# Optimization experiments

Hardware: AMD Instinct MI355X
Metric: run time of the kernel (lower is better)

The kernel has to match this reference:

```python
import jax, jax.numpy as jnp
import numpy as np

B, T, D, H = 4, 2048, 1024, 64

def setup_inputs() -> dict:
    key = jax.random.key(0)
    kx, kq, kk, kv = jax.random.split(key, 4)
    s = 1.0 / np.sqrt(D)
    return {
        "x": jax.random.normal(kx, (B, T, D), dtype=jnp.float32),
        "Wq": jax.random.normal(kq, (D, H), dtype=jnp.float32) * s,
        "Wk": jax.random.normal(kk, (D, H), dtype=jnp.float32) * s,
        "Wv": jax.random.normal(kv, (D, H), dtype=jnp.float32) * s,
    }

def reference(x, Wq, Wk, Wv):
    # q,k,v: [B,T,H]
    q = jnp.einsum('btd,dh->bth', x, Wq)
    k = jnp.einsum('btd,dh->bth', x, Wk)
    v = jnp.einsum('btd,dh->bth', x, Wv)
    scale = jnp.asarray(H, x.dtype) ** -0.5
    wei = jnp.einsum('bqh,bkh->bqk', q, k) * scale  # [B,T,T]
    Tlen = x.shape[1]
    causal = jnp.tril(jnp.ones((Tlen, Tlen), dtype=bool))
    wei = jnp.where(causal, wei, -jnp.inf)
    attn = jax.nn.softmax(wei, axis=-1)
    return jnp.einsum('bqk,bkh->bqh', attn, v)
```

## Files before the change

kernel.cpp:

```cpp
#include <hip/hip_runtime.h>
#include <hip/hip_bf16.h>
#include <math.h>

#define Bb   4
#define Tlen 2048
#define Dd   1024
#define Hh   64
#define NROWS 8192
#define NQ   32
#define NC   4

typedef short bf16x8 __attribute__((ext_vector_type(8)));
typedef float f32x4  __attribute__((ext_vector_type(4)));

__device__ __forceinline__ unsigned short f2b(float f) {
    unsigned u = __float_as_uint(f);
    unsigned r = u + 0x7FFFu + ((u >> 16) & 1u);
    return (unsigned short)(r >> 16);
}
__device__ __forceinline__ unsigned pk2(float a, float b) {
    __hip_bfloat162 h = __float22bfloat162_rn(make_float2(a, b));
    return *reinterpret_cast<unsigned*>(&h);
}

__global__ __launch_bounds__(256) void wtrans_kernel(
    const float* __restrict__ Wq, const float* __restrict__ Wk,
    const float* __restrict__ Wv, unsigned short* __restrict__ wfrag)
{
    const int s = blockIdx.x * 256 + threadIdx.x;
    const int f   = s / 768;
    const int rem = s % 768;
    const int nb  = rem >> 6;
    const int lane = rem & 63;
    const int g = lane >> 4, qr = lane & 15;
    const int n = nb * 16 + qr;
    const int wsel = n >> 6, h = n & 63;
    const float* W = (wsel == 0) ? Wq : (wsel == 1) ? Wk : Wv;
    const int k0 = (f >> 1) * 64 + (f & 1) * 32 + g * 8;
    unsigned short tmp[8];
    #pragma unroll
    for (int j = 0; j < 8; ++j) tmp[j] = f2b(W[(size_t)(k0 + j) * Hh + h]);
    *(bf16x8*)(wfrag + (size_t)s * 8) = *(const bf16x8*)tmp;
}

__global__ __launch_bounds__(256) void proj_kernel(
    const float* __restrict__ x, const unsigned short* __restrict__ wfrag,
    unsigned short* __restrict__ qw, unsigned short* __restrict__ kfr,
    unsigned short* __restrict__ vfr)
{
    __shared__ unsigned short xs[2][32 * 64];

    const int rb   = blockIdx.x * 32;
    const int tid  = threadIdx.x;
    const int wv   = tid >> 6;
    const int lane = tid & 63;
    const int qr   = lane & 15;
    const int g    = lane >> 4;

    const int xr = tid >> 3, xc8 = tid & 7;
    const float* xg0 = x + (size_t)(rb + xr) * Dd + xc8 * 8;

    const unsigned short* wp = wfrag + ((size_t)(wv * 3) * 64 + lane) * 8;

    f32x4 acc[6] = {};

    float4 px0 = *(const float4*)(xg0 + 0);
    float4 px1 = *(const float4*)(xg0 + 4);

    bf16x8 wr[6];
    #pragma unroll
    for (int ks = 0; ks < 2; ++ks)
        #pragma unroll
        for (int nf = 0; nf < 3; ++nf)
            wr[ks * 3 + nf] = *(const bf16x8*)(wp + (size_t)(ks * 12 + nf) * 512);

    #pragma unroll
    for (int t = 0; t < 16; ++t) {
        const int cur = t & 1;
        {
            union { unsigned u[4]; bf16x8 v; } p8;
            p8.u[0] = pk2(px0.x, px0.y);
            p8.u[1] = pk2(px0.z, px0.w);
            p8.u[2] = pk2(px1.x, px1.y);
            p8.u[3] = pk2(px1.z, px1.w);
            *(bf16x8*)(&xs[cur][xr * 64 + ((xc8 ^ (xr & 7)) << 3)]) = p8.v;
        }
        __syncthreads();

        bf16x8 wn[6];
        if (t < 15) {
            px0 = *(const float4*)(xg0 + (t + 1) * 64 + 0);
            px1 = *(const float4*)(xg0 + (t + 1) * 64 + 4);
            const int fb = (t + 1) * 2;
            #pragma unroll
            for (int ks = 0; ks < 2; ++ks)
                #pragma unroll
                for (int nf = 0; nf < 3; ++nf)
                    wn[ks * 3 + nf] = *(const bf16x8*)(wp + (size_t)((fb + ks) * 12 + nf) * 512);
        }

        #pragma unroll
        for (int ks = 0; ks < 2; ++ks) {
            #pragma unroll
            for (int mf = 0; mf < 2; ++mf) {
                const int arow = mf * 16 + qr;
                const bf16x8 a = *(const bf16x8*)(
                    &xs[cur][arow * 64 + (((ks * 4 + g) ^ (arow & 7)) << 3)]);
                acc[mf * 3 + 0] = __builtin_amdgcn_mfma_f32_16x16x32_bf16(a, wr[ks * 3 + 0], acc[mf * 3 + 0], 0, 0, 0);
                acc[mf * 3 + 1] = __builtin_amdgcn_mfma_f32_16x16x32_bf16(a, wr[ks * 3 + 1], acc[mf * 3 + 1], 0, 0, 0);
                acc[mf * 3 + 2] = __builtin_amdgcn_mfma_f32_16x16x32_bf16(a, wr[ks * 3 + 2], acc[mf * 3 + 2], 0, 0, 0);
            }
        }
        __syncthreads();

        if (t < 15) {
            #pragma unroll
            for (int i = 0; i < 6; ++i) wr[i] = wn[i];
        }
    }

    #pragma unroll
    for (int mf = 0; mf < 2; ++mf) {
        #pragma unroll
        for (int nf0 = 0; nf0 < 3; ++nf0) {
            const int n = wv * 48 + nf0 * 16 + qr;
            const int wsel = n >> 6, h = n & 63;
            const f32x4 ov = acc[mf * 3 + nf0];
            #pragma unroll
            for (int r = 0; r < 4; ++r) {
                const int row = rb + mf * 16 + 4 * g + r;
                const unsigned short val = f2b(ov[r]);
                if (wsel == 0) {
                    qw[(size_t)row * Hh + h] = val;
                } else if (wsel == 1) {
                    const int bq = row >> 11, t = row & 2047;
                    const int t16 = t >> 4, qrk = t & 15;
                    const int ks = h >> 5, gk = (h >> 3) & 3, e = h & 7;
                    kfr[((((size_t)bq * 128 + t16) * 2 + ks) * 64 + gk * 16 + qrk) * 8 + e] = val;
                } else {
                    const int bq = row >> 11, t = row & 2047;
                    const int kt = t >> 5, jj = t & 31;
                    const int gv = jj >> 3, e = jj & 7;
                    const int nfv = h >> 4, qrv = h & 15;
                    vfr[((((size_t)bq * 64 + kt) * 4 + nfv) * 64 + gv * 16 + qrv) * 8 + e] = val;
                }
            }
        }
    }
}

__global__ __launch_bounds__(256) void attn_kernel(
    const unsigned short* __restrict__ qw, const unsigned short* __restrict__ kfr,
    const unsigned short* __restrict__ vfr,
    float* __restrict__ part_O, float* __restrict__ part_ml)
{
    const int qt = (NQ - 1) - blockIdx.x;
    const int ci = blockIdx.y;
    const int b  = blockIdx.z;
    const int tid = threadIdx.x;
    const int wv = tid >> 6, lane = tid & 63;
    const int qr = lane & 15, g = lane >> 4;

    const int ntk = 2 * qt + 2;
    const int tpc = (ntk + NC - 1) / NC;
    const int t0  = ci * tpc;
    const int t1  = (ntk < t0 + tpc) ? ntk : (t0 + tpc);

    const size_t base = (size_t)b * Tlen * Hh;
    const unsigned short* kfb = kfr + (size_t)b * 131072 + lane * 8;
    const unsigned short* vfb = vfr + (size_t)b * 131072 + lane * 8;
    const int qrow = qt * 64 + wv * 16 + qr;

    const bf16x8 qf0 = *(const bf16x8*)(qw + base + (size_t)qrow * Hh + 8 * g);
    const bf16x8 qf1 = *(const bf16x8*)(qw + base + (size_t)qrow * Hh + 32 + 8 * g);

    f32x4 o0 = {}, o1 = {}, o2 = {}, o3 = {};
    float m = -INFINITY, l = 0.f;

    bf16x8 kf[4], vf[4];
    if (t0 < t1) {
        #pragma unroll
        for (int i = 0; i < 4; ++i) {
            kf[i] = *(const bf16x8*)(kfb + (size_t)(t0 * 4 + i) * 512);
            vf[i] = *(const bf16x8*)(vfb + (size_t)(t0 * 4 + i) * 512);
        }
    }

    for (int kt = t0; kt < t1; ++kt) {
        const int j0 = kt * 32;

        bf16x8 kn[4], vn[4];
        if (kt + 1 < t1) {
            #pragma unroll
            for (int i = 0; i < 4; ++i) {
                kn[i] = *(const bf16x8*)(kfb + (size_t)((kt + 1) * 4 + i) * 512);
                vn[i] = *(const bf16x8*)(vfb + (size_t)((kt + 1) * 4 + i) * 512);
            }
        }

        f32x4 a0 = {}, a1 = {};
        a0 = __builtin_amdgcn_mfma_f32_16x16x32_bf16(kf[0], qf0, a0, 0, 0, 0);
        a0 = __builtin_amdgcn_mfma_f32_16x16x32_bf16(kf[1], qf1, a0, 0, 0, 0);
        a1 = __builtin_amdgcn_mfma_f32_16x16x32_bf16(kf[2], qf0, a1, 0, 0, 0);
        a1 = __builtin_amdgcn_mfma_f32_16x16x32_bf16(kf[3], qf1, a1, 0, 0, 0);

        float p[8];
        float tm = -INFINITY;
        #pragma unroll
        for (int jf = 0; jf < 2; ++jf) {
            #pragma unroll
            for (int r = 0; r < 4; ++r) {
                const int jg = j0 + jf * 16 + 4 * g + r;
                float s = ((jf == 0) ? a0[r] : a1[r]) * 0.125f;
                s = (jg > qrow) ? -INFINITY : s;
                p[jf * 4 + r] = s;
                tm = fmaxf(tm, s);
            }
        }
        tm = fmaxf(tm, __shfl_xor(tm, 16));
        tm = fmaxf(tm, __shfl_xor(tm, 32));
        const float mnew = fmaxf(m, tm);
        const float mc   = fmaxf(mnew, -1e30f);
        float psum = 0.f;
        #pragma unroll
        for (int i = 0; i < 8; ++i) {
            const float pv = __expf(p[i] - mc);
            p[i] = pv; psum += pv;
        }
        psum += __shfl_xor(psum, 16);
        psum += __shfl_xor(psum, 32);

        if (!__all(tm <= m)) {
            const float alpha = (m == -INFINITY) ? 0.f : __expf(m - mc);
            const float ar0 = __shfl(alpha, 4 * g + 0);
            const float ar1 = __shfl(alpha, 4 * g + 1);
            const float ar2 = __shfl(alpha, 4 * g + 2);
            const float ar3 = __shfl(alpha, 4 * g + 3);
            o0[0] *= ar0; o0[1] *= ar1; o0[2] *= ar2; o0[3] *= ar3;
            o1[0] *= ar0; o1[1] *= ar1; o1[2] *= ar2; o1[3] *= ar3;
            o2[0] *= ar0; o2[1] *= ar1; o2[2] *= ar2; o2[3] *= ar3;
            o3[0] *= ar0; o3[1] *= ar1; o3[2] *= ar2; o3[3] *= ar3;
            l = l * alpha + psum;
        } else {
            l += psum;
        }
        m = mnew;

        unsigned pw[4];
        pw[0] = f2b(p[0]) | ((unsigned)f2b(p[1]) << 16);
        pw[1] = f2b(p[2]) | ((unsigned)f2b(p[3]) << 16);
        pw[2] = f2b(p[4]) | ((unsigned)f2b(p[5]) << 16);
        pw[3] = f2b(p[6]) | ((unsigned)f2b(p[7]) << 16);
        union PU { unsigned u[4]; bf16x8 v; } pu;
        #pragma unroll
        for (int w = 0; w < 4; ++w) {
            const int gp  = 2 * g + (w >> 1);
            const int src = 16 * (gp & 3) + qr;
            const unsigned t0s = __shfl(pw[0 + (w & 1)], src);
            const unsigned t1s = __shfl(pw[2 + (w & 1)], src);
            pu.u[w] = (gp & 4) ? t1s : t0s;
        }
        const bf16x8 pa = pu.v;

        o0 = __builtin_amdgcn_mfma_f32_16x16x32_bf16(pa, vf[0], o0, 0, 0, 0);
        o1 = __builtin_amdgcn_mfma_f32_16x16x32_bf16(pa, vf[1], o1, 0, 0, 0);
        o2 = __builtin_amdgcn_mfma_f32_16x16x32_bf16(pa, vf[2], o2, 0, 0, 0);
        o3 = __builtin_amdgcn_mfma_f32_16x16x32_bf16(pa, vf[3], o3, 0, 0, 0);

        if (kt + 1 < t1) {
            #pragma unroll
            for (int i = 0; i < 4; ++i) { kf[i] = kn[i]; vf[i] = vn[i]; }
        }
    }

    const int blin = (b * NQ + qt) * NC + ci;
    float* po = part_O + (size_t)blin * 4096;
    #pragma unroll
    for (int nf = 0; nf < 4; ++nf) {
        const f32x4 ov = (nf == 0) ? o0 : (nf == 1) ? o1 : (nf == 2) ? o2 : o3;
        #pragma unroll
        for (int r = 0; r < 4; ++r)
            po[(size_t)(wv * 16 + 4 * g + r) * 64 + nf * 16 + qr] = ov[r];
    }
    if (g == 0) {
        part_ml[(size_t)blin * 128 + wv * 16 + qr]      = m;
        part_ml[(size_t)blin * 128 + 64 + wv * 16 + qr] = l;
    }
}

__global__ __launch_bounds__(256) void merge_kernel(
    const float* __restrict__ part_O, const float* __restrict__ part_ml,
    float* __restrict__ out)
{
    const int idx = blockIdx.x * 256 + threadIdx.x;
    const int row = idx >> 6;
    const int c   = idx & 63;
    const int b   = row >> 11;
    const int t   = row & 2047;
    const int qt  = t >> 6;
    const int qq  = t & 63;
    const int bl0 = (b * NQ + qt) * NC;

    float M = -INFINITY;
    #pragma unroll
    for (int i = 0; i < NC; ++i) {
        const float lvi = part_ml[(size_t)(bl0 + i) * 128 + 64 + qq];
        if (lvi > 0.f) M = fmaxf(M, part_ml[(size_t)(bl0 + i) * 128 + qq]);
    }
    float num = 0.f, den = 0.f;
    #pragma unroll
    for (int i = 0; i < NC; ++i) {
        const float lvi = part_ml[(size_t)(bl0 + i) * 128 + 64 + qq];
        if (lvi > 0.f) {
            const float wgt = __expf(part_ml[(size_t)(bl0 + i) * 128 + qq] - M);
            num += wgt * part_O[(size_t)(bl0 + i) * 4096 + (size_t)qq * 64 + c];
            den += wgt * lvi;
        }
    }
    out[(size_t)row * 64 + c] = num / den;
}

extern "C" void kernel_launch(void* const* d_in, const int* in_sizes, int n_in,
                              void* d_out, int out_size, void* d_ws, size_t ws_size,
                              hipStream_t stream) {
    const float* x  = (const float*)d_in[0];
    const float* Wq = (const float*)d_in[1];
    const float* Wk = (const float*)d_in[2];
    const float* Wv = (const float*)d_in[3];
    float* outp = (float*)d_out;

    unsigned short* wfrag = (unsigned short*)d_ws;
    unsigned short* qw  = wfrag + 192 * 1024;
    unsigned short* kfr = qw + NROWS * Hh;
    unsigned short* vfr = kfr + NROWS * Hh;
    float* part_O  = (float*)(vfr + NROWS * Hh);
    float* part_ml = part_O + (size_t)(Bb * NQ * NC) * 4096;

    wtrans_kernel<<<dim3(96), 256, 0, stream>>>(Wq, Wk, Wv, wfrag);
    proj_kernel<<<dim3(NROWS / 32), 256, 0, stream>>>(x, wfrag, qw, kfr, vfr);
    attn_kernel<<<dim3(NQ, NC, Bb), 256, 0, stream>>>(qw, kfr, vfr, part_O, part_ml);
    merge_kernel<<<dim3((NROWS * Hh) / 256), 256, 0, stream>>>(part_O, part_ml, outp);
}
```

Baseline: 46.67 us.

## Use 64-key tiles with adaptive split-K chunking and unmasked off-diagonal path

The attention kernel now processes 64 keys per iteration instead of 32, doubling the MFMA work per softmax/shuffle round. The split-K chunk count per query tile becomes adaptive (up to 8) rather than a fixed 4, and blocks with no work exit early. The causal mask is applied only on the diagonal tile. The merge kernel is updated to match. Risks include higher register pressure from 16-element score arrays and 8 V fragments, V no longer being prefetched a tile ahead, and more partial results to merge.

```diff
diff --git a/kernel.cpp b/kernel.cpp
--- a/kernel.cpp
+++ b/kernel.cpp
@@ -8,7 +8,7 @@
 #define Hh   64
 #define NROWS 8192
 #define NQ   32
-#define NC   4
+#define MAXCH 8
 
 typedef short bf16x8 __attribute__((ext_vector_type(8)));
 typedef float f32x4  __attribute__((ext_vector_type(4)));
@@ -157,14 +157,18 @@
     const int qt = (NQ - 1) - blockIdx.x;
     const int ci = blockIdx.y;
     const int b  = blockIdx.z;
+
+    const int ntk = qt + 1;
+    const int nch = min(MAXCH, (ntk + 1) >> 1);
+    const int C   = (ntk + nch - 1) / nch;
+    const int nuse = (ntk + C - 1) / C;
+    if (ci >= nuse) return;
+    const int t0 = ci * C;
+    const int t1 = (ntk < t0 + C) ? ntk : (t0 + C);
+
     const int tid = threadIdx.x;
     const int wv = tid >> 6, lane = tid & 63;
     const int qr = lane & 15, g = lane >> 4;
-
-    const int ntk = 2 * qt + 2;
-    const int tpc = (ntk + NC - 1) / NC;
-    const int t0  = ci * tpc;
-    const int t1  = (ntk < t0 + tpc) ? ntk : (t0 + tpc);
 
     const size_t base = (size_t)b * Tlen * Hh;
     const unsigned short* kfb = kfr + (size_t)b * 131072 + lane * 8;
@@ -174,48 +178,58 @@
     const bf16x8 qf0 = *(const bf16x8*)(qw + base + (size_t)qrow * Hh + 8 * g);
     const bf16x8 qf1 = *(const bf16x8*)(qw + base + (size_t)qrow * Hh + 32 + 8 * g);
 
-    f32x4 o0 = {}, o1 = {}, o2 = {}, o3 = {};
+    f32x4 o[4] = {};
     float m = -INFINITY, l = 0.f;
 
-    bf16x8 kf[4], vf[4];
-    if (t0 < t1) {
-        #pragma unroll
-        for (int i = 0; i < 4; ++i) {
-            kf[i] = *(const bf16x8*)(kfb + (size_t)(t0 * 4 + i) * 512);
-            vf[i] = *(const bf16x8*)(vfb + (size_t)(t0 * 4 + i) * 512);
-        }
-    }
+    bf16x8 kf[8];
+    #pragma unroll
+    for (int i = 0; i < 8; ++i)
+        kf[i] = *(const bf16x8*)(kfb + (size_t)(t0 * 8 + i) * 512);
 
     for (int kt = t0; kt < t1; ++kt) {
-        const int j0 = kt * 32;
-
-        bf16x8 kn[4], vn[4];
+        const int j0 = kt * 64;
+
+        bf16x8 vf[8];
+        #pragma unroll
+        for (int i = 0; i < 8; ++i)
+            vf[i] = *(const bf16x8*)(vfb + (size_t)(kt * 8 + i) * 512);
+
+        f32x4 a[4] = {};
+        #pragma unroll
+        for (int jf = 0; jf < 4; ++jf) {
+            a[jf] = __builtin_amdgcn_mfma_f32_16x16x32_bf16(kf[jf * 2 + 0], qf0, a[jf], 0, 0, 0);
+            a[jf] = __builtin_amdgcn_mfma_f32_16x16x32_bf16(kf[jf * 2 + 1], qf1, a[jf], 0, 0, 0);
+        }
+
+        bf16x8 kn[8];
         if (kt + 1 < t1) {
             #pragma unroll
-            for (int i = 0; i < 4; ++i) {
-                kn[i] = *(const bf16x8*)(kfb + (size_t)((kt + 1) * 4 + i) * 512);
-                vn[i] = *(const bf16x8*)(vfb + (size_t)((kt + 1) * 4 + i) * 512);
-            }
-        }
-
-        f32x4 a0 = {}, a1 = {};
-        a0 = __builtin_amdgcn_mfma_f32_16x16x32_bf16(kf[0], qf0, a0, 0, 0, 0);
-        a0 = __builtin_amdgcn_mfma_f32_16x16x32_bf16(kf[1], qf1, a0, 0, 0, 0);
-        a1 = __builtin_amdgcn_mfma_f32_16x16x32_bf16(kf[2], qf0, a1, 0, 0, 0);
-        a1 = __builtin_amdgcn_mfma_f32_16x16x32_bf16(kf[3], qf1, a1, 0, 0, 0);
-
-        float p[8];
+            for (int i = 0; i < 8; ++i)
+                kn[i] = *(const bf16x8*)(kfb + (size_t)((kt + 1) * 8 + i) * 512);
+        }
+
+        float p[16];
         float tm = -INFINITY;
-        #pragma unroll
-        for (int jf = 0; jf < 2; ++jf) {
-            #pragma unroll
-            for (int r = 0; r < 4; ++r) {
-                const int jg = j0 + jf * 16 + 4 * g + r;
-                float s = ((jf == 0) ? a0[r] : a1[r]) * 0.125f;
-                s = (jg > qrow) ? -INFINITY : s;
-                p[jf * 4 + r] = s;
-                tm = fmaxf(tm, s);
-            }
+        if (kt == qt) {
+            #pragma unroll
+            for (int jf = 0; jf < 4; ++jf)
+                #pragma unroll
+                for (int r = 0; r < 4; ++r) {
+                    const int jg = j0 + jf * 16 + 4 * g + r;
+                    float s = a[jf][r] * 0.125f;
+                    s = (jg > qrow) ? -INFINITY : s;
+                    p[jf * 4 + r] = s;
+                    tm = fmaxf(tm, s);
+                }
+        } else {
+            #pragma unroll
+            for (int jf = 0; jf < 4; ++jf)
+                #pragma unroll
+                for (int r = 0; r < 4; ++r) {
+                    const float s = a[jf][r] * 0.125f;
+                    p[jf * 4 + r] = s;
+                    tm = fmaxf(tm, s);
+                }
         }
         tm = fmaxf(tm, __shfl_xor(tm, 16));
         tm = fmaxf(tm, __shfl_xor(tm, 32));
@@ -223,7 +237,7 @@
         const float mc   = fmaxf(mnew, -1e30f);
         float psum = 0.f;
         #pragma unroll
-        for (int i = 0; i < 8; ++i) {
+        for (int i = 0; i < 16; ++i) {
             const float pv = __expf(p[i] - mc);
             p[i] = pv; psum += pv;
         }
@@ -236,51 +250,54 @@
             const float ar1 = __shfl(alpha, 4 * g + 1);
             const float ar2 = __shfl(alpha, 4 * g + 2);
             const float ar3 = __shfl(alpha, 4 * g + 3);
-            o0[0] *= ar0; o0[1] *= ar1; o0[2] *= ar2; o0[3] *= ar3;
-            o1[0] *= ar0; o1[1] *= ar1; o1[2] *= ar2; o1[3] *= ar3;
-            o2[0] *= ar0; o2[1] *= ar1; o2[2] *= ar2; o2[3] *= ar3;
-            o3[0] *= ar0; o3[1] *= ar1; o3[2] *= ar2; o3[3] *= ar3;
+            #pragma unroll
+            for (int nf = 0; nf < 4; ++nf) {
+                o[nf][0] *= ar0; o[nf][1] *= ar1; o[nf][2] *= ar2; o[nf][3] *= ar3;
+            }
             l = l * alpha + psum;
         } else {
             l += psum;
         }
         m = mnew;
 
-        unsigned pw[4];
-        pw[0] = f2b(p[0]) | ((unsigned)f2b(p[1]) << 16);
-        pw[1] = f2b(p[2]) | ((unsigned)f2b(p[3]) << 16);
-        pw[2] = f2b(p[4]) | ((unsigned)f2b(p[5]) << 16);
-        pw[3] = f2b(p[6]) | ((unsigned)f2b(p[7]) << 16);
-        union PU { unsigned u[4]; bf16x8 v; } pu;
+        unsigned pw[8];
+        #pragma unroll
+        for (int jf = 0; jf < 4; ++jf) {
+            pw[jf * 2 + 0] = f2b(p[jf * 4 + 0]) | ((unsigned)f2b(p[jf * 4 + 1]) << 16);
+            pw[jf * 2 + 1] = f2b(p[jf * 4 + 2]) | ((unsigned)f2b(p[jf * 4 + 3]) << 16);
+        }
+        union PU { unsigned u[4]; bf16x8 v; } pl, ph;
         #pragma unroll
         for (int w = 0; w < 4; ++w) {
-            const int gp  = 2 * g + (w >> 1);
-            const int src = 16 * (gp & 3) + qr;
-            const unsigned t0s = __shfl(pw[0 + (w & 1)], src);
-            const unsigned t1s = __shfl(pw[2 + (w & 1)], src);
-            pu.u[w] = (gp & 4) ? t1s : t0s;
-        }
-        const bf16x8 pa = pu.v;
-
-        o0 = __builtin_amdgcn_mfma_f32_16x16x32_bf16(pa, vf[0], o0, 0, 0, 0);
-        o1 = __builtin_amdgcn_mfma_f32_16x16x32_bf16(pa, vf[1], o1, 0, 0, 0);
-        o2 = __builtin_amdgcn_mfma_f32_16x16x32_bf16(pa, vf[2], o2, 0, 0, 0);
-        o3 = __builtin_amdgcn_mfma_f32_16x16x32_bf16(pa, vf[3], o3, 0, 0, 0);
+            const int src = 16 * ((g & 1) * 2 + (w >> 1)) + qr;
+            const unsigned s0 = __shfl(pw[0 + (w & 1)], src);
+            const unsigned s1 = __shfl(pw[2 + (w & 1)], src);
+            const unsigned s2 = __shfl(pw[4 + (w & 1)], src);
+            const unsigned s3 = __shfl(pw[6 + (w & 1)], src);
+            pl.u[w] = (g >> 1) ? s1 : s0;
+            ph.u[w] = (g >> 1) ? s3 : s2;
+        }
+        const bf16x8 pa0 = pl.v, pa1 = ph.v;
+
+        #pragma unroll
+        for (int nf = 0; nf < 4; ++nf) {
+            o[nf] = __builtin_amdgcn_mfma_f32_16x16x32_bf16(pa0, vf[0 * 4 + nf], o[nf], 0, 0, 0);
+            o[nf] = __builtin_amdgcn_mfma_f32_16x16x32_bf16(pa1, vf[1 * 4 + nf], o[nf], 0, 0, 0);
+        }
 
         if (kt + 1 < t1) {
             #pragma unroll
-            for (int i = 0; i < 4; ++i) { kf[i] = kn[i]; vf[i] = vn[i]; }
-        }
-    }
-
-    const int blin = (b * NQ + qt) * NC + ci;
+            for (int i = 0; i < 8; ++i) kf[i] = kn[i];
+        }
+    }
+
+    const int blin = (b * NQ + qt) * MAXCH + ci;
     float* po = part_O + (size_t)blin * 4096;
     #pragma unroll
     for (int nf = 0; nf < 4; ++nf) {
-        const f32x4 ov = (nf == 0) ? o0 : (nf == 1) ? o1 : (nf == 2) ? o2 : o3;
         #pragma unroll
         for (int r = 0; r < 4; ++r)
-            po[(size_t)(wv * 16 + 4 * g + r) * 64 + nf * 16 + qr] = ov[r];
+            po[(size_t)(wv * 16 + 4 * g + r) * 64 + nf * 16 + qr] = o[nf][r];
     }
     if (g == 0) {
         part_ml[(size_t)blin * 128 + wv * 16 + qr]      = m;
@@ -299,23 +316,22 @@
     const int t   = row & 2047;
     const int qt  = t >> 6;
     const int qq  = t & 63;
-    const int bl0 = (b * NQ + qt) * NC;
+
+    const int ntk = qt + 1;
+    const int nch = min(MAXCH, (ntk + 1) >> 1);
+    const int C   = (ntk + nch - 1) / nch;
+    const int nuse = (ntk + C - 1) / C;
+    const int bl0 = (b * NQ + qt) * MAXCH;
 
     float M = -INFINITY;
-    #pragma unroll
-    for (int i = 0; i < NC; ++i) {
+    for (int i = 0; i < nuse; ++i)
+        M = fmaxf(M, part_ml[(size_t)(bl0 + i) * 128 + qq]);
+    float num = 0.f, den = 0.f;
+    for (int i = 0; i < nuse; ++i) {
         const float lvi = part_ml[(size_t)(bl0 + i) * 128 + 64 + qq];
-        if (lvi > 0.f) M = fmaxf(M, part_ml[(size_t)(bl0 + i) * 128 + qq]);
-    }
-    float num = 0.f, den = 0.f;
-    #pragma unroll
-    for (int i = 0; i < NC; ++i) {
-        const float lvi = part_ml[(size_t)(bl0 + i) * 128 + 64 + qq];
-        if (lvi > 0.f) {
-            const float wgt = __expf(part_ml[(size_t)(bl0 + i) * 128 + qq] - M);
-            num += wgt * part_O[(size_t)(bl0 + i) * 4096 + (size_t)qq * 64 + c];
-            den += wgt * lvi;
-        }
+        const float wgt = __expf(part_ml[(size_t)(bl0 + i) * 128 + qq] - M);
+        num += wgt * part_O[(size_t)(bl0 + i) * 4096 + (size_t)qq * 64 + c];
+        den += wgt * lvi;
     }
     out[(size_t)row * 64 + c] = num / den;
 }
@@ -334,10 +350,10 @@
     unsigned short* kfr = qw + NROWS * Hh;
     unsigned short* vfr = kfr + NROWS * Hh;
     float* part_O  = (float*)(vfr + NROWS * Hh);
-    float* part_ml = part_O + (size_t)(Bb * NQ * NC) * 4096;
+    float* part_ml = part_O + (size_t)(Bb * NQ * MAXCH) * 4096;
 
     wtrans_kernel<<<dim3(96), 256, 0, stream>>>(Wq, Wk, Wv, wfrag);
     proj_kernel<<<dim3(NROWS / 32), 256, 0, stream>>>(x, wfrag, qw, kfr, vfr);
-    attn_kernel<<<dim3(NQ, NC, Bb), 256, 0, stream>>>(qw, kfr, vfr, part_O, part_ml);
+    attn_kernel<<<dim3(NQ, MAXCH, Bb), 256, 0, stream>>>(qw, kfr, vfr, part_O, part_ml);
     merge_kernel<<<dim3((NROWS * Hh) / 256), 256, 0, stream>>>(part_O, part_ml, outp);
 }
```

Result: no change. 46.44 us (-0.5%).
